# Kernel optimization log

Hardware: AMD Instinct MI355X
Metric: run time of the kernel (lower is better)

## Reference

```python
import jax, jax.numpy as jnp
import numpy as np

MUL0, MUL1 = 128, 64
DIM1 = MUL0 + 3 * MUL1          # 320 = dim of 128x0e + 64x1o
DIM2 = 4                        # 1x0e + 1x1o
WDIM, H = 16, 64
# per-instruction weight sizes (mul_in2 = 1), e3nn instruction order
N1 = MUL0 * MUL0                # (0e x 0e -> 0e)
N2 = MUL0 * MUL1                # (0e x 1o -> 1o)
N3 = MUL1 * MUL1                # (1o x 0e -> 1o)
N4 = MUL1 * MUL0                # (1o x 1o -> 0e)
WNUMEL = N1 + N2 + N3 + N4      # 36864
FAN = MUL0 + MUL1               # summed fan-in per output slice = 192
PW0 = float(np.sqrt(1.0 / FAN))         # path weight, component/element norm, l_out=0
PW1 = float(np.sqrt(3.0 / FAN))         # l_out=1 (alpha = 2l+1 = 3)
INV_SQRT3 = float(1.0 / np.sqrt(3.0))   # wigner_3j(1,1,0)/(0,1,1)/(1,0,1) entries
SQRT_K = float(1.0 / np.sqrt(FAN))      # tp_rescale correction (output divided by this)


def setup_inputs() -> dict:
    key = jax.random.key(0)
    ks = jax.random.split(key, 8)
    N = 4096

    def lin(k, fin, fout):
        k1, k2 = jax.random.split(k)
        lim = 1.0 / np.sqrt(fin)
        W = jax.random.uniform(k1, (fin, fout), minval=-lim, maxval=lim, dtype=jnp.float32)
        b = jax.random.uniform(k2, (fout,), minval=-lim, maxval=lim, dtype=jnp.float32)
        return W, b

    W0, b0 = lin(ks[3], WDIM, H)
    W1, b1 = lin(ks[4], H, H)
    W2, b2 = lin(ks[5], H, WNUMEL)
    return {
        "data_in1": jax.random.normal(ks[0], (N, DIM1), dtype=jnp.float32),
        "data_in2": jax.random.normal(ks[1], (N, DIM2), dtype=jnp.float32),
        "weight": jax.random.normal(ks[2], (N, WDIM), dtype=jnp.float32),
        "W0": W0, "b0": b0, "W1": W1, "b1": b1, "W2": W2, "b2": b2,
        "bias": jax.random.uniform(ks[6], (MUL0,), minval=-SQRT_K, maxval=SQRT_K, dtype=jnp.float32),
    }


def _forward(data_in1, data_in2, weight, W0, b0, W1, b1, W2, b2, bias):
    # weight-generating MLP: 16 -> 64 -> 64 -> weight_numel
    h = jax.nn.relu(weight @ W0 + b0)
    h = jax.nn.relu(h @ W1 + b1)
    w = h @ W2 + b2                                   # [N, WNUMEL] per-sample tp weights
    # split inputs into irrep blocks
    s1 = data_in1[:, :MUL0]                           # [N,128]  128x0e
    v1 = data_in1[:, MUL0:].reshape(-1, MUL1, 3)      # [N,64,3]  64x1o
    s2 = data_in2[:, 0]                               # [N]       1x0e
    v2 = data_in2[:, 1:4]                             # [N,3]     1x1o
    # per-instruction weight views (uvw with v=1 collapsed)
    Wa = w[:, :N1].reshape(-1, MUL0, MUL0)                   # 0e x 0e -> 0e
    Wb = w[:, N1:N1 + N2].reshape(-1, MUL0, MUL1)            # 0e x 1o -> 1o
    Wc = w[:, N1 + N2:N1 + N2 + N3].reshape(-1, MUL1, MUL1)  # 1o x 0e -> 1o
    Wd = w[:, N1 + N2 + N3:].reshape(-1, MUL1, MUL0)         # 1o x 1o -> 0e
    dot12 = jnp.einsum('eui,ei->eu', v1, v2)          # [N,64]
    # scalar (0e) output slice: paths Wa (w3j=1) and Wd (w3j = delta/sqrt(3))
    out0 = PW0 * (jnp.einsum('euw,eu->ew', Wa, s1) * s2[:, None]
                  + INV_SQRT3 * jnp.einsum('euw,eu->ew', Wd, dot12))
    # vector (1o) output slice: paths Wb and Wc (w3j = delta/sqrt(3))
    out1 = PW1 * INV_SQRT3 * (
        jnp.einsum('euw,eu->ew', Wb, s1)[:, :, None] * v2[:, None, :]
        + jnp.einsum('euw,eui->ewi', Wc, v1) * s2[:, None, None])
    out = jnp.concatenate([out0, out1.reshape(-1, 3 * MUL1)], axis=1)  # [N,320]
    out = out / SQRT_K                                # tp_rescale: divide by sqrt_k correction
    out = out.at[:, :MUL0].add(bias)                  # bias added on 0e slice only
    return out


def reference(data_in1, data_in2, weight, W0, b0, W1, b1, W2, b2, bias):
    return _forward(data_in1, data_in2, weight, W0, b0, W1, b1, W2, b2, bias)
```

## Files before the change

### kernel.cpp

```cpp
#include <hip/hip_runtime.h>
#include <hip/hip_bf16.h>

typedef __attribute__((ext_vector_type(8))) short short8;
typedef __attribute__((ext_vector_type(4))) float f32x4;
typedef __attribute__((ext_vector_type(4))) unsigned uint4v;

constexpr int N1 = 16384, N2 = 8192, N3 = 4096;
constexpr int WN = 36864;
constexpr float ISQ3 = 0.57735026918962576451f;

__device__ __forceinline__ unsigned short f2bf(float f) {
  unsigned u = __builtin_bit_cast(unsigned, f);
  u += 0x7fffu + ((u >> 16) & 1u);
  return (unsigned short)(u >> 16);
}

__device__ __forceinline__ unsigned pkbf(float a, float b) {
  unsigned r;
  asm("v_cvt_pk_bf16_f32 %0, %1, %2" : "=v"(r) : "v"(a), "v"(b));
  return r;
}

#define MFMA(a, b, c) __builtin_amdgcn_mfma_f32_16x16x32_bf16((a), (b), (c), 0, 0, 0)

#define CVT8(X0, X1, G) do { uint4v w_;                                       \
    w_[0] = pkbf(X0[0], X0[1]); w_[1] = pkbf(X0[2], X0[3]);                   \
    w_[2] = pkbf(X1[0], X1[1]); w_[3] = pkbf(X1[2], X1[3]);                   \
    G = __builtin_bit_cast(short8, w_); } while (0)

#define LOADH(EF, LO, HI) do {                                                \
    const float* hp_ = H + (size_t)(e0 + 16 * (EF) + nl) * 64 + grp * 8;      \
    f32x4 x0_ = *(const f32x4*)hp_,        x1_ = *(const f32x4*)(hp_ + 4);    \
    f32x4 x2_ = *(const f32x4*)(hp_ + 32), x3_ = *(const f32x4*)(hp_ + 36);   \
    CVT8(x0_, x1_, LO); CVT8(x2_, x3_, HI); } while (0)

__global__ __launch_bounds__(256)
void k_prep(const float* __restrict__ wgt, const float* __restrict__ W0,
            const float* __restrict__ b0, const float* __restrict__ W1,
            const float* __restrict__ b1, const float* __restrict__ W2,
            const float* __restrict__ d1, const float* __restrict__ d2,
            float* __restrict__ H, unsigned short* __restrict__ Bp,
            float* __restrict__ sBg, float* __restrict__ sDg,
            float* __restrict__ sCg, float* __restrict__ d2T) {
  __shared__ __align__(16) float shm[10400];
  const int bid = blockIdx.x;
  const int tid = threadIdx.x;

  if (bid < 288) {
    const int n0 = bid * 128;
#pragma unroll
    for (int q = 0; q < 8; ++q) {
      const int flat = tid + q * 256;
      const int row = flat >> 5, c4 = flat & 31;
      *(f32x4*)&shm[row * 132 + c4 * 4] =
          *(const f32x4*)(W2 + (size_t)row * WN + n0 + c4 * 4);
    }
    __syncthreads();
#pragma unroll
    for (int q = 0; q < 4; ++q) {
      const int p = tid + q * 256;
      const int ntl = p >> 7, kh = (p >> 6) & 1, lane2 = p & 63;
      const int k0 = kh * 32 + (lane2 >> 4) * 8;
      const int col = ntl * 16 + (lane2 & 15);
      short8 v;
#pragma unroll
      for (int qq = 0; qq < 8; ++qq) v[qq] = (short)f2bf(shm[(k0 + qq) * 132 + col]);
      *(short8*)(Bp + ((size_t)(n0 * 8 + p)) * 8) = v;
    }
  } else if (bid < 1312) {
    float* h0s = shm;
    const int r = tid >> 6, jj = tid & 63;
    const int e = (bid - 288) * 4 + r;
    float a = b0[jj];
#pragma unroll
    for (int i = 0; i < 16; ++i) a = fmaf(wgt[e * 16 + i], W0[i * 64 + jj], a);
    h0s[r * 64 + jj] = fmaxf(a, 0.f);
    __syncthreads();
    float a1 = b1[jj];
#pragma unroll
    for (int i = 0; i < 64; ++i) a1 = fmaf(h0s[r * 64 + i], W1[i * 64 + jj], a1);
    H[e * 64 + jj] = fmaxf(a1, 0.f);
  } else {
    float* d1s = shm;
    float* d2s = shm + 10272;
    const int e0 = (bid - 1312) * 32;
    for (int x = tid; x < 32 * 320; x += 256) {
      int e = x / 320, c = x % 320;
      d1s[e * 321 + c] = d1[(size_t)(e0 + e) * 320 + c];
    }
    if (tid < 128) d2s[tid] = d2[(size_t)e0 * 4 + tid];
    __syncthreads();
    const int e = tid & 31;
    const float s2 = d2s[e * 4 + 0];
    const float w1 = d2s[e * 4 + 1], w2 = d2s[e * 4 + 2], w3 = d2s[e * 4 + 3];
    for (int row = 128 + (tid >> 5); row < 516; row += 8) {
      float v; float* dst;
      if (row < 256)      { v = d1s[e * 321 + (row - 128)];            dst = sBg + (size_t)(row - 128) * 4096; }
      else if (row < 320) { int u = row - 256;
        v = ISQ3 * (d1s[e * 321 + 128 + 3 * u] * w1 + d1s[e * 321 + 129 + 3 * u] * w2 +
                    d1s[e * 321 + 130 + 3 * u] * w3);                  dst = sDg + (size_t)u * 4096; }
      else if (row < 512) { v = d1s[e * 321 + 128 + (row - 320)] * s2; dst = sCg + (size_t)(row - 320) * 4096; }
      else                { v = d2s[e * 4 + (row - 512)];              dst = d2T + (size_t)(row - 512) * 4096; }
      dst[e0 + e] = v;
    }
  }
}

__global__ __launch_bounds__(512, 4)
void k_main(const float* __restrict__ sBg, const float* __restrict__ sDg,
            const float* __restrict__ sCg, const float* __restrict__ d2T,
            const float* __restrict__ H, const unsigned short* __restrict__ Bp,
            const float* __restrict__ b2, const float* __restrict__ bias,
            float* __restrict__ out) {
  __shared__ __align__(16) float buf[8448];
  const int bid = blockIdx.x, tid = threadIdx.x;
  const int wid = tid >> 6, lane = tid & 63;
  const int nl = lane & 15, grp = lane >> 4;
  const short8* Bp8 = (const short8*)Bp;
  const f32x4 Zv = {0.f, 0.f, 0.f, 0.f};

  if (bid < 512) {
    const int j = bid & 7;
    const int e0 = (bid >> 3) * 64;
    short8 hL0, hH0, hL1, hH1, hL2, hH2, hL3, hH3;
    LOADH(0, hL0, hH0);
    LOADH(1, hL1, hH1);
    LOADH(2, hL2, hH2);
    LOADH(3, hL3, hH3);

    f32x4 aA0 = Zv, aA1 = Zv, aA2 = Zv, aA3 = Zv;
    f32x4 aD0 = Zv, aD1 = Zv, aD2 = Zv, aD3 = Zv;

    {
      const int u0 = wid * 16;
      const short8* pa = Bp8 + (size_t)(u0 * 8 + j) * 128 + lane;
      const float* sb = sBg + (size_t)u0 * 4096 + e0 + nl;
      const float* pb = b2 + (size_t)u0 * 128 + 16 * j + 4 * grp;
      short8 F0 = pa[0], F1 = pa[64];
      f32x4 bv = *(const f32x4*)pb;
      float s0 = sb[0], s1 = sb[16], s2 = sb[32], s3 = sb[48];
#pragma unroll
      for (int t = 0; t < 16; ++t) {
        short8 f0 = F0, f1 = F1; f32x4 b = bv;
        float c0 = s0, c1 = s1, c2 = s2, c3 = s3;
        if (t < 15) {
          pa += 1024; sb += 4096; pb += 128;
          F0 = pa[0]; F1 = pa[64]; bv = *(const f32x4*)pb;
          s0 = sb[0]; s1 = sb[16]; s2 = sb[32]; s3 = sb[48];
        }
        f32x4 tt;
        tt = MFMA(f0, hL0, b); tt = MFMA(f1, hH0, tt); aA0 += c0 * tt;
        tt = MFMA(f0, hL1, b); tt = MFMA(f1, hH1, tt); aA1 += c1 * tt;
        tt = MFMA(f0, hL2, b); tt = MFMA(f1, hH2, tt); aA2 += c2 * tt;
        tt = MFMA(f0, hL3, b); tt = MFMA(f1, hH3, tt); aA3 += c3 * tt;
      }
    }
    {
      const int u0 = wid * 8;
      const short8* pa = Bp8 + (size_t)(1792 + u0 * 8 + j) * 128 + lane;
      const float* sd = sDg + (size_t)u0 * 4096 + e0 + nl;
      const float* pb = b2 + (size_t)(N1 + N2 + N3) + (size_t)u0 * 128 + 16 * j + 4 * grp;
      short8 F0 = pa[0], F1 = pa[64];
      f32x4 bv = *(const f32x4*)pb;
      float s0 = sd[0], s1 = sd[16], s2 = sd[32], s3 = sd[48];
#pragma unroll
      for (int t = 0; t < 8; ++t) {
        short8 f0 = F0, f1 = F1; f32x4 b = bv;
        float c0 = s0, c1 = s1, c2 = s2, c3 = s3;
        if (t < 7) {
          pa += 1024; sd += 4096; pb += 128;
          F0 = pa[0]; F1 = pa[64]; bv = *(const f32x4*)pb;
          s0 = sd[0]; s1 = sd[16]; s2 = sd[32]; s3 = sd[48];
        }
        f32x4 tt;
        tt = MFMA(f0, hL0, b); tt = MFMA(f1, hH0, tt); aD0 += c0 * tt;
        tt = MFMA(f0, hL1, b); tt = MFMA(f1, hH1, tt); aD1 += c1 * tt;
        tt = MFMA(f0, hL2, b); tt = MFMA(f1, hH2, tt); aD2 += c2 * tt;
        tt = MFMA(f0, hL3, b); tt = MFMA(f1, hH3, tt); aD3 += c3 * tt;
      }
    }
    {
      float* bw = &buf[(wid & 3) * 2112];
      if (wid >= 4) {
#pragma unroll
        for (int r = 0; r < 4; ++r) {
          bw[nl * 33 + grp * 4 + r]             = aA0[r];
          bw[(16 + nl) * 33 + grp * 4 + r]      = aA1[r];
          bw[(32 + nl) * 33 + grp * 4 + r]      = aA2[r];
          bw[(48 + nl) * 33 + grp * 4 + r]      = aA3[r];
          bw[nl * 33 + 16 + grp * 4 + r]        = aD0[r];
          bw[(16 + nl) * 33 + 16 + grp * 4 + r] = aD1[r];
          bw[(32 + nl) * 33 + 16 + grp * 4 + r] = aD2[r];
          bw[(48 + nl) * 33 + 16 + grp * 4 + r] = aD3[r];
        }
      }
      __syncthreads();
      if (wid < 4) {
#pragma unroll
        for (int r = 0; r < 4; ++r) {
          bw[nl * 33 + grp * 4 + r]             += aA0[r];
          bw[(16 + nl) * 33 + grp * 4 + r]      += aA1[r];
          bw[(32 + nl) * 33 + grp * 4 + r]      += aA2[r];
          bw[(48 + nl) * 33 + grp * 4 + r]      += aA3[r];
          bw[nl * 33 + 16 + grp * 4 + r]        += aD0[r];
          bw[(16 + nl) * 33 + 16 + grp * 4 + r] += aD1[r];
          bw[(32 + nl) * 33 + 16 + grp * 4 + r] += aD2[r];
          bw[(48 + nl) * 33 + 16 + grp * 4 + r] += aD3[r];
        }
      }
      __syncthreads();
#pragma unroll
      for (int it = 0; it < 2; ++it) {
        const int p = tid + it * 512;
        const int e = p >> 4, w = p & 15;
        float ta = buf[e * 33 + w] + buf[2112 + e * 33 + w] +
                   buf[4224 + e * 33 + w] + buf[6336 + e * 33 + w];
        float td = buf[e * 33 + 16 + w] + buf[2112 + e * 33 + 16 + w] +
                   buf[4224 + e * 33 + 16 + w] + buf[6336 + e * 33 + 16 + w];
        out[(size_t)(e0 + e) * 320 + 16 * j + w] = d2T[e0 + e] * ta + td + bias[16 * j + w];
      }
    }
  } else {
    const int idx = bid - 512;
    const int xcd = idx & 7;
    const int jc = xcd & 3;
    const int tile = ((idx >> 3) << 1) | (xcd >> 2);
    const int e0 = tile * 32;
    short8 gL0, gH0, gL1, gH1;
    LOADH(0, gL0, gH0);
    LOADH(1, gL1, gH1);

    f32x4 aB0 = Zv, aB1 = Zv;
    f32x4 c00 = Zv, c01 = Zv, c02 = Zv, c10 = Zv, c11 = Zv, c12 = Zv;

    {
      const int u0 = wid * 16;
      const short8* pa = Bp8 + (size_t)(1024 + u0 * 4 + jc) * 128 + lane;
      const float* sb = sBg + (size_t)u0 * 4096 + e0 + nl;
      const float* pb = b2 + (size_t)N1 + (size_t)u0 * 64 + 16 * jc + 4 * grp;
      short8 F0 = pa[0], F1 = pa[64];
      f32x4 bv = *(const f32x4*)pb;
      float s0 = sb[0], s1 = sb[16];
#pragma unroll
      for (int t = 0; t < 16; ++t) {
        short8 f0 = F0, f1 = F1; f32x4 b = bv;
        float c0 = s0, c1 = s1;
        if (t < 15) {
          pa += 512; sb += 4096; pb += 64;
          F0 = pa[0]; F1 = pa[64]; bv = *(const f32x4*)pb;
          s0 = sb[0]; s1 = sb[16];
        }
        f32x4 tt;
        tt = MFMA(f0, gL0, b); tt = MFMA(f1, gH0, tt); aB0 += c0 * tt;
        tt = MFMA(f0, gL1, b); tt = MFMA(f1, gH1, tt); aB1 += c1 * tt;
      }
    }
    {
      const int u0 = wid * 8;
      const short8* pa = Bp8 + (size_t)(1536 + u0 * 4 + jc) * 128 + lane;
      const float* sc = sCg + (size_t)(3 * u0) * 4096 + e0 + nl;
      const float* pb = b2 + (size_t)(N1 + N2) + (size_t)u0 * 64 + 16 * jc + 4 * grp;
      short8 F0 = pa[0], F1 = pa[64];
      f32x4 bv = *(const f32x4*)pb;
      float s00 = sc[0], s01 = sc[16];
      float s10 = sc[4096], s11 = sc[4096 + 16];
      float s20 = sc[8192], s21 = sc[8192 + 16];
#pragma unroll
      for (int t = 0; t < 8; ++t) {
        short8 f0 = F0, f1 = F1; f32x4 b = bv;
        float d00 = s00, d01 = s01, d10 = s10, d11 = s11, d20 = s20, d21 = s21;
        if (t < 7) {
          pa += 512; sc += 12288; pb += 64;
          F0 = pa[0]; F1 = pa[64]; bv = *(const f32x4*)pb;
          s00 = sc[0]; s01 = sc[16];
          s10 = sc[4096]; s11 = sc[4096 + 16];
          s20 = sc[8192]; s21 = sc[8192 + 16];
        }
        f32x4 t0 = MFMA(f0, gL0, b); t0 = MFMA(f1, gH0, t0);
        f32x4 t1 = MFMA(f0, gL1, b); t1 = MFMA(f1, gH1, t1);
        c00 += d00 * t0; c01 += d10 * t0; c02 += d20 * t0;
        c10 += d01 * t1; c11 += d11 * t1; c12 += d21 * t1;
      }
    }
    {
      float* bw = &buf[(wid & 3) * 2080];
      if (wid >= 4) {
#pragma unroll
        for (int r = 0; r < 4; ++r) {
          const int w1 = grp * 4 + r;
          bw[nl * 65 + w1]             = aB0[r];
          bw[(16 + nl) * 65 + w1]      = aB1[r];
          bw[nl * 65 + 16 + w1]        = c00[r];
          bw[nl * 65 + 32 + w1]        = c01[r];
          bw[nl * 65 + 48 + w1]        = c02[r];
          bw[(16 + nl) * 65 + 16 + w1] = c10[r];
          bw[(16 + nl) * 65 + 32 + w1] = c11[r];
          bw[(16 + nl) * 65 + 48 + w1] = c12[r];
        }
      }
      __syncthreads();
      if (wid < 4) {
#pragma unroll
        for (int r = 0; r < 4; ++r) {
          const int w1 = grp * 4 + r;
          bw[nl * 65 + w1]             += aB0[r];
          bw[(16 + nl) * 65 + w1]      += aB1[r];
          bw[nl * 65 + 16 + w1]        += c00[r];
          bw[nl * 65 + 32 + w1]        += c01[r];
          bw[nl * 65 + 48 + w1]        += c02[r];
          bw[(16 + nl) * 65 + 16 + w1] += c10[r];
          bw[(16 + nl) * 65 + 32 + w1] += c11[r];
          bw[(16 + nl) * 65 + 48 + w1] += c12[r];
        }
      }
      __syncthreads();
#pragma unroll
      for (int it = 0; it < 3; ++it) {
        const int p = tid + it * 512;
        const int e = p / 48, rem = p % 48;
        const int w1 = rem / 3, i = rem % 3;
        float tb = buf[e * 65 + w1] + buf[2080 + e * 65 + w1] +
                   buf[4160 + e * 65 + w1] + buf[6240 + e * 65 + w1];
        const int co = 16 + i * 16 + w1;
        float tc = buf[e * 65 + co] + buf[2080 + e * 65 + co] +
                   buf[4160 + e * 65 + co] + buf[6240 + e * 65 + co];
        out[(size_t)(e0 + e) * 320 + 128 + (size_t)(16 * jc + w1) * 3 + i] =
            tb * d2T[(1 + i) * 4096 + e0 + e] + tc;
      }
    }
  }
}

extern "C" void kernel_launch(void* const* d_in, const int* in_sizes, int n_in,
                              void* d_out, int out_size, void* d_ws, size_t ws_size,
                              hipStream_t stream) {
  const float* d1   = (const float*)d_in[0];
  const float* d2   = (const float*)d_in[1];
  const float* wgt  = (const float*)d_in[2];
  const float* W0   = (const float*)d_in[3];
  const float* b0   = (const float*)d_in[4];
  const float* W1   = (const float*)d_in[5];
  const float* b1   = (const float*)d_in[6];
  const float* W2   = (const float*)d_in[7];
  const float* b2   = (const float*)d_in[8];
  const float* bias = (const float*)d_in[9];
  float* out = (float*)d_out;

  char* ws = (char*)d_ws;
  float* H           = (float*)(ws);
  unsigned short* Bp = (unsigned short*)(ws + (1u << 20));
  float* sBg         = (float*)(ws + (8u << 20));
  float* sDg         = (float*)(ws + (10u << 20));
  float* sCg         = (float*)(ws + (11u << 20));
  float* d2T         = (float*)(ws + (14u << 20));

  k_prep<<<1440, 256, 0, stream>>>(wgt, W0, b0, W1, b1, W2, d1, d2,
                                   H, Bp, sBg, sDg, sCg, d2T);
  k_main<<<1024, 512, 0, stream>>>(sBg, sDg, sCg, d2T, H, Bp, b2, bias, out);
}
```

Baseline: 68.61 us.

## Halve k_main block to 4 waves with 3-deep register prefetch ring

Shrinks k_main blocks from 512 to 256 threads, so each of 4 waves handles twice the reduction range (u) and the two-stage LDS partial-sum reduction becomes a single store, sync and 4-way sum. The single-buffer next-iteration prefetch is replaced with a 3-slot register ring that keeps loads three iterations ahead, hiding global-load latency behind the MFMA chains. This costs more registers per wave, and occupancy falls with launch bounds (256,3) and half as many waves per block.

New measurement: 65.07 us. 5.2% less time.

```diff
diff --git a/kernel.cpp b/kernel.cpp
--- a/kernel.cpp
+++ b/kernel.cpp
@@ -106,7 +106,7 @@
   }
 }
 
-__global__ __launch_bounds__(512, 4)
+__global__ __launch_bounds__(256, 3)
 void k_main(const float* __restrict__ sBg, const float* __restrict__ sDg,
             const float* __restrict__ sCg, const float* __restrict__ d2T,
             const float* __restrict__ H, const unsigned short* __restrict__ Bp,
@@ -132,21 +132,29 @@
     f32x4 aD0 = Zv, aD1 = Zv, aD2 = Zv, aD3 = Zv;
 
     {
-      const int u0 = wid * 16;
+      const int u0 = wid * 32;
       const short8* pa = Bp8 + (size_t)(u0 * 8 + j) * 128 + lane;
       const float* sb = sBg + (size_t)u0 * 4096 + e0 + nl;
       const float* pb = b2 + (size_t)u0 * 128 + 16 * j + 4 * grp;
-      short8 F0 = pa[0], F1 = pa[64];
-      f32x4 bv = *(const f32x4*)pb;
-      float s0 = sb[0], s1 = sb[16], s2 = sb[32], s3 = sb[48];
-#pragma unroll
-      for (int t = 0; t < 16; ++t) {
-        short8 f0 = F0, f1 = F1; f32x4 b = bv;
-        float c0 = s0, c1 = s1, c2 = s2, c3 = s3;
-        if (t < 15) {
+      short8 Fa[3], Fb[3]; f32x4 Bv[3];
+      float S0[3], S1[3], S2[3], S3[3];
+#pragma unroll
+      for (int q = 0; q < 3; ++q) {
+        Fa[q] = pa[0]; Fb[q] = pa[64];
+        Bv[q] = *(const f32x4*)pb;
+        S0[q] = sb[0]; S1[q] = sb[16]; S2[q] = sb[32]; S3[q] = sb[48];
+        pa += 1024; sb += 4096; pb += 128;
+      }
+#pragma unroll
+      for (int t = 0; t < 32; ++t) {
+        const int s = t % 3;
+        short8 f0 = Fa[s], f1 = Fb[s]; f32x4 b = Bv[s];
+        float c0 = S0[s], c1 = S1[s], c2 = S2[s], c3 = S3[s];
+        if (t < 29) {
+          Fa[s] = pa[0]; Fb[s] = pa[64];
+          Bv[s] = *(const f32x4*)pb;
+          S0[s] = sb[0]; S1[s] = sb[16]; S2[s] = sb[32]; S3[s] = sb[48];
           pa += 1024; sb += 4096; pb += 128;
-          F0 = pa[0]; F1 = pa[64]; bv = *(const f32x4*)pb;
-          s0 = sb[0]; s1 = sb[16]; s2 = sb[32]; s3 = sb[48];
         }
         f32x4 tt;
         tt = MFMA(f0, hL0, b); tt = MFMA(f1, hH0, tt); aA0 += c0 * tt;
@@ -156,21 +164,29 @@
       }
     }
     {
-      const int u0 = wid * 8;
+      const int u0 = wid * 16;
       const short8* pa = Bp8 + (size_t)(1792 + u0 * 8 + j) * 128 + lane;
       const float* sd = sDg + (size_t)u0 * 4096 + e0 + nl;
       const float* pb = b2 + (size_t)(N1 + N2 + N3) + (size_t)u0 * 128 + 16 * j + 4 * grp;
-      short8 F0 = pa[0], F1 = pa[64];
-      f32x4 bv = *(const f32x4*)pb;
-      float s0 = sd[0], s1 = sd[16], s2 = sd[32], s3 = sd[48];
-#pragma unroll
-      for (int t = 0; t < 8; ++t) {
-        short8 f0 = F0, f1 = F1; f32x4 b = bv;
-        float c0 = s0, c1 = s1, c2 = s2, c3 = s3;
-        if (t < 7) {
+      short8 Fa[3], Fb[3]; f32x4 Bv[3];
+      float S0[3], S1[3], S2[3], S3[3];
+#pragma unroll
+      for (int q = 0; q < 3; ++q) {
+        Fa[q] = pa[0]; Fb[q] = pa[64];
+        Bv[q] = *(const f32x4*)pb;
+        S0[q] = sd[0]; S1[q] = sd[16]; S2[q] = sd[32]; S3[q] = sd[48];
+        pa += 1024; sd += 4096; pb += 128;
+      }
+#pragma unroll
+      for (int t = 0; t < 16; ++t) {
+        const int s = t % 3;
+        short8 f0 = Fa[s], f1 = Fb[s]; f32x4 b = Bv[s];
+        float c0 = S0[s], c1 = S1[s], c2 = S2[s], c3 = S3[s];
+        if (t < 13) {
+          Fa[s] = pa[0]; Fb[s] = pa[64];
+          Bv[s] = *(const f32x4*)pb;
+          S0[s] = sd[0]; S1[s] = sd[16]; S2[s] = sd[32]; S3[s] = sd[48];
           pa += 1024; sd += 4096; pb += 128;
-          F0 = pa[0]; F1 = pa[64]; bv = *(const f32x4*)pb;
-          s0 = sd[0]; s1 = sd[16]; s2 = sd[32]; s3 = sd[48];
         }
         f32x4 tt;
         tt = MFMA(f0, hL0, b); tt = MFMA(f1, hH0, tt); aD0 += c0 * tt;
@@ -180,38 +196,22 @@
       }
     }
     {
-      float* bw = &buf[(wid & 3) * 2112];
-      if (wid >= 4) {
-#pragma unroll
-        for (int r = 0; r < 4; ++r) {
-          bw[nl * 33 + grp * 4 + r]             = aA0[r];
-          bw[(16 + nl) * 33 + grp * 4 + r]      = aA1[r];
-          bw[(32 + nl) * 33 + grp * 4 + r]      = aA2[r];
-          bw[(48 + nl) * 33 + grp * 4 + r]      = aA3[r];
-          bw[nl * 33 + 16 + grp * 4 + r]        = aD0[r];
-          bw[(16 + nl) * 33 + 16 + grp * 4 + r] = aD1[r];
-          bw[(32 + nl) * 33 + 16 + grp * 4 + r] = aD2[r];
-          bw[(48 + nl) * 33 + 16 + grp * 4 + r] = aD3[r];
-        }
+      float* bw = &buf[wid * 2112];
+#pragma unroll
+      for (int r = 0; r < 4; ++r) {
+        bw[nl * 33 + grp * 4 + r]             = aA0[r];
+        bw[(16 + nl) * 33 + grp * 4 + r]      = aA1[r];
+        bw[(32 + nl) * 33 + grp * 4 + r]      = aA2[r];
+        bw[(48 + nl) * 33 + grp * 4 + r]      = aA3[r];
+        bw[nl * 33 + 16 + grp * 4 + r]        = aD0[r];
+        bw[(16 + nl) * 33 + 16 + grp * 4 + r] = aD1[r];
+        bw[(32 + nl) * 33 + 16 + grp * 4 + r] = aD2[r];
+        bw[(48 + nl) * 33 + 16 + grp * 4 + r] = aD3[r];
       }
       __syncthreads();
-      if (wid < 4) {
-#pragma unroll
-        for (int r = 0; r < 4; ++r) {
-          bw[nl * 33 + grp * 4 + r]             += aA0[r];
-          bw[(16 + nl) * 33 + grp * 4 + r]      += aA1[r];
-          bw[(32 + nl) * 33 + grp * 4 + r]      += aA2[r];
-          bw[(48 + nl) * 33 + grp * 4 + r]      += aA3[r];
-          bw[nl * 33 + 16 + grp * 4 + r]        += aD0[r];
-          bw[(16 + nl) * 33 + 16 + grp * 4 + r] += aD1[r];
-          bw[(32 + nl) * 33 + 16 + grp * 4 + r] += aD2[r];
-          bw[(48 + nl) * 33 + 16 + grp * 4 + r] += aD3[r];
-        }
-      }
-      __syncthreads();
-#pragma unroll
-      for (int it = 0; it < 2; ++it) {
-        const int p = tid + it * 512;
+#pragma unroll
+      for (int it = 0; it < 4; ++it) {
+        const int p = tid + it * 256;
         const int e = p >> 4, w = p & 15;
         float ta = buf[e * 33 + w] + buf[2112 + e * 33 + w] +
                    buf[4224 + e * 33 + w] + buf[6336 + e * 33 + w];
@@ -234,21 +234,29 @@
     f32x4 c00 = Zv, c01 = Zv, c02 = Zv, c10 = Zv, c11 = Zv, c12 = Zv;
 
     {
-      const int u0 = wid * 16;
+      const int u0 = wid * 32;
       const short8* pa = Bp8 + (size_t)(1024 + u0 * 4 + jc) * 128 + lane;
       const float* sb = sBg + (size_t)u0 * 4096 + e0 + nl;
       const float* pb = b2 + (size_t)N1 + (size_t)u0 * 64 + 16 * jc + 4 * grp;
-      short8 F0 = pa[0], F1 = pa[64];
-      f32x4 bv = *(const f32x4*)pb;
-      float s0 = sb[0], s1 = sb[16];
-#pragma unroll
-      for (int t = 0; t < 16; ++t) {
-        short8 f0 = F0, f1 = F1; f32x4 b = bv;
-        float c0 = s0, c1 = s1;
-        if (t < 15) {
+      short8 Fa[3], Fb[3]; f32x4 Bv[3];
+      float S0[3], S1[3];
+#pragma unroll
+      for (int q = 0; q < 3; ++q) {
+        Fa[q] = pa[0]; Fb[q] = pa[64];
+        Bv[q] = *(const f32x4*)pb;
+        S0[q] = sb[0]; S1[q] = sb[16];
+        pa += 512; sb += 4096; pb += 64;
+      }
+#pragma unroll
+      for (int t = 0; t < 32; ++t) {
+        const int s = t % 3;
+        short8 f0 = Fa[s], f1 = Fb[s]; f32x4 b = Bv[s];
+        float c0 = S0[s], c1 = S1[s];
+        if (t < 29) {
+          Fa[s] = pa[0]; Fb[s] = pa[64];
+          Bv[s] = *(const f32x4*)pb;
+          S0[s] = sb[0]; S1[s] = sb[16];
           pa += 512; sb += 4096; pb += 64;
-          F0 = pa[0]; F1 = pa[64]; bv = *(const f32x4*)pb;
-          s0 = sb[0]; s1 = sb[16];
         }
         f32x4 tt;
         tt = MFMA(f0, gL0, b); tt = MFMA(f1, gH0, tt); aB0 += c0 * tt;
@@ -256,25 +264,33 @@
       }
     }
     {
-      const int u0 = wid * 8;
+      const int u0 = wid * 16;
       const short8* pa = Bp8 + (size_t)(1536 + u0 * 4 + jc) * 128 + lane;
       const float* sc = sCg + (size_t)(3 * u0) * 4096 + e0 + nl;
       const float* pb = b2 + (size_t)(N1 + N2) + (size_t)u0 * 64 + 16 * jc + 4 * grp;
-      short8 F0 = pa[0], F1 = pa[64];
-      f32x4 bv = *(const f32x4*)pb;
-      float s00 = sc[0], s01 = sc[16];
-      float s10 = sc[4096], s11 = sc[4096 + 16];
-      float s20 = sc[8192], s21 = sc[8192 + 16];
-#pragma unroll
-      for (int t = 0; t < 8; ++t) {
-        short8 f0 = F0, f1 = F1; f32x4 b = bv;
-        float d00 = s00, d01 = s01, d10 = s10, d11 = s11, d20 = s20, d21 = s21;
-        if (t < 7) {
+      short8 Fa[3], Fb[3]; f32x4 Bv[3];
+      float S00[3], S01[3], S10[3], S11[3], S20[3], S21[3];
+#pragma unroll
+      for (int q = 0; q < 3; ++q) {
+        Fa[q] = pa[0]; Fb[q] = pa[64];
+        Bv[q] = *(const f32x4*)pb;
+        S00[q] = sc[0]; S01[q] = sc[16];
+        S10[q] = sc[4096]; S11[q] = sc[4096 + 16];
+        S20[q] = sc[8192]; S21[q] = sc[8192 + 16];
+        pa += 512; sc += 12288; pb += 64;
+      }
+#pragma unroll
+      for (int t = 0; t < 16; ++t) {
+        const int s = t % 3;
+        short8 f0 = Fa[s], f1 = Fb[s]; f32x4 b = Bv[s];
+        float d00 = S00[s], d01 = S01[s], d10 = S10[s], d11 = S11[s], d20 = S20[s], d21 = S21[s];
+        if (t < 13) {
+          Fa[s] = pa[0]; Fb[s] = pa[64];
+          Bv[s] = *(const f32x4*)pb;
+          S00[s] = sc[0]; S01[s] = sc[16];
+          S10[s] = sc[4096]; S11[s] = sc[4096 + 16];
+          S20[s] = sc[8192]; S21[s] = sc[8192 + 16];
           pa += 512; sc += 12288; pb += 64;
-          F0 = pa[0]; F1 = pa[64]; bv = *(const f32x4*)pb;
-          s00 = sc[0]; s01 = sc[16];
-          s10 = sc[4096]; s11 = sc[4096 + 16];
-          s20 = sc[8192]; s21 = sc[8192 + 16];
         }
         f32x4 t0 = MFMA(f0, gL0, b); t0 = MFMA(f1, gH0, t0);
         f32x4 t1 = MFMA(f0, gL1, b); t1 = MFMA(f1, gH1, t1);
@@ -283,40 +299,23 @@
       }
     }
     {
-      float* bw = &buf[(wid & 3) * 2080];
-      if (wid >= 4) {
-#pragma unroll
-        for (int r = 0; r < 4; ++r) {
-          const int w1 = grp * 4 + r;
-          bw[nl * 65 + w1]             = aB0[r];
-          bw[(16 + nl) * 65 + w1]      = aB1[r];
-          bw[nl * 65 + 16 + w1]        = c00[r];
-          bw[nl * 65 + 32 + w1]        = c01[r];
-          bw[nl * 65 + 48 + w1]        = c02[r];
-          bw[(16 + nl) * 65 + 16 + w1] = c10[r];
-          bw[(16 + nl) * 65 + 32 + w1] = c11[r];
-          bw[(16 + nl) * 65 + 48 + w1] = c12[r];
-        }
+      float* bw = &buf[wid * 2080];
+#pragma unroll
+      for (int r = 0; r < 4; ++r) {
+        const int w1 = grp * 4 + r;
+        bw[nl * 65 + w1]             = aB0[r];
+        bw[(16 + nl) * 65 + w1]      = aB1[r];
+        bw[nl * 65 + 16 + w1]        = c00[r];
+        bw[nl * 65 + 32 + w1]        = c01[r];
+        bw[nl * 65 + 48 + w1]        = c02[r];
+        bw[(16 + nl) * 65 + 16 + w1] = c10[r];
+        bw[(16 + nl) * 65 + 32 + w1] = c11[r];
+        bw[(16 + nl) * 65 + 48 + w1] = c12[r];
       }
       __syncthreads();
-      if (wid < 4) {
-#pragma unroll
-        for (int r = 0; r < 4; ++r) {
-          const int w1 = grp * 4 + r;
-          bw[nl * 65 + w1]             += aB0[r];
-          bw[(16 + nl) * 65 + w1]      += aB1[r];
-          bw[nl * 65 + 16 + w1]        += c00[r];
-          bw[nl * 65 + 32 + w1]        += c01[r];
-          bw[nl * 65 + 48 + w1]        += c02[r];
-          bw[(16 + nl) * 65 + 16 + w1] += c10[r];
-          bw[(16 + nl) * 65 + 32 + w1] += c11[r];
-          bw[(16 + nl) * 65 + 48 + w1] += c12[r];
-        }
-      }
-      __syncthreads();
-#pragma unroll
-      for (int it = 0; it < 3; ++it) {
-        const int p = tid + it * 512;
+#pragma unroll
+      for (int it = 0; it < 6; ++it) {
+        const int p = tid + it * 256;
         const int e = p / 48, rem = p % 48;
         const int w1 = rem / 3, i = rem % 3;
         float tb = buf[e * 65 + w1] + buf[2080 + e * 65 + w1] +
@@ -356,5 +355,5 @@
 
   k_prep<<<1440, 256, 0, stream>>>(wgt, W0, b0, W1, b1, W2, d1, d2,
                                    H, Bp, sBg, sDg, sCg, d2T);
-  k_main<<<1024, 512, 0, stream>>>(sBg, sDg, sCg, d2T, H, Bp, b2, bias, out);
-}
+  k_main<<<1024, 256, 0, stream>>>(sBg, sDg, sCg, d2T, H, Bp, b2, bias, out);
+}
```
